# Performance work log

Hardware: AMD Instinct MI355X
Metric: run time of the kernel (lower is better)

Reference implementation:

```python
import jax, jax.numpy as jnp
import numpy as np

B, S, T, D, N, V = 16, 4, 1000, 256, 8192, 50000
EPS = 2.220446049250313e-16  # sys.float_info.epsilon


def setup_inputs() -> dict:
    key = jax.random.key(0)
    ks = jax.random.split(key, 10)
    spks = jax.random.normal(ks[0], (B, S, T, D), jnp.float32)   # frame-level speaker vectors
    ys = jax.random.uniform(ks[1], (B, T, S), jnp.float32)        # predictions (unused in math)
    ts = jax.random.uniform(ks[2], (B, T, S), jnp.float32)        # soft targets / weights
    ss = jax.random.randint(ks[3], (B, S), 0, N)                  # candidate index per speaker
    sigmas = jnp.argsort(jax.random.uniform(ks[4], (B, S)), axis=1)  # per-sample permutation
    ns = jax.random.randint(ks[5], (B, N), 0, V)                  # candidate speaker ids
    ilens = jax.random.randint(ks[6], (B,), T // 2, T + 1)        # valid frame counts
    table = jax.random.normal(ks[7], (V, D), jnp.float32)         # nn.Embedding weight
    alpha = jax.random.uniform(ks[8], (), jnp.float32) + 0.5
    beta = jax.random.uniform(ks[9], (), jnp.float32) + 0.5
    return {"spks": spks, "ys": ys, "ts": ts, "ss": ss, "sigmas": sigmas,
            "ns": ns, "ilens": ilens, "table": table, "alpha": alpha, "beta": beta}


def reference(spks, ys, ts, ss, sigmas, ns, ilens, table, alpha, beta):
    # frame validity mask [B,T]
    mask = (jnp.arange(T)[None, :] < ilens[:, None]).astype(spks.dtype)
    # per-frame L2 normalize speaker vectors: [B,S,T,D]
    nspk = spks / jnp.linalg.norm(spks, axis=-1, keepdims=True)
    # weights w[b,s,t] = ts[b, t, sigma[b,s]]
    w_raw = jnp.take_along_axis(ts, sigmas[:, None, :], axis=2)  # [B,T,S]
    w_raw = jnp.transpose(w_raw, (0, 2, 1))                      # [B,S,T]
    w = w_raw * mask[:, None, :]
    # weighted average over valid frames, then normalize: [B,S,D]
    wavg = jnp.einsum('bst,bstd->bsd', w, nspk)
    e = wavg / jnp.linalg.norm(wavg, axis=-1, keepdims=True)
    # gather + normalize candidate embeddings: [B,N,D]
    emb = table[ns]
    emb = emb / jnp.linalg.norm(emb, axis=-1, keepdims=True)
    # squared euclidean distance between unit vectors: dist^2 = 2 - 2 cos
    dist2 = jnp.maximum(2.0 - 2.0 * jnp.einsum('bsd,bnd->bsn', e, emb), 0.0)
    d = jnp.maximum(alpha, EPS) * dist2 + beta                   # [B,S,N]
    logp = jax.nn.log_softmax(-d, axis=-1)
    idx = jnp.take_along_axis(ss, sigmas, axis=1)                # s[sigma[spkid]] -> [B,S]
    loss_bs = -jnp.take_along_axis(logp, idx[:, :, None], axis=-1)[..., 0]  # [B,S]
    # speaker active iff sum of rounded targets over valid frames > 0
    active = jnp.sum(jnp.round(w_raw) * mask[:, None, :], axis=-1) > 0
    loss_bs = jnp.where(active, loss_bs, 0.0)
    return jnp.mean(loss_bs)
```

## Files before the change

### kernel.cpp

```cpp
#include <hip/hip_runtime.h>
#include <math.h>

#define B_ 16
#define S_ 4
#define T_ 1000
#define D_ 256
#define N_ 8192
#define V_ 50000

constexpr int NC1 = 20;
constexpr int TC1 = (T_ + NC1 - 1) / NC1;
constexpr int NCSE = 32;
constexpr int CPSE = N_ / NCSE;
constexpr int GNB  = (V_ + 63) / 64;

constexpr size_t OFF_W   = 0;
constexpr size_t OFF_CNT = OFF_W   + (size_t)64*NC1*D_;
constexpr size_t OFF_E   = OFF_CNT + (size_t)64*NC1;
constexpr size_t OFF_IDX = OFF_E   + (size_t)64*D_;
constexpr size_t OFF_ACT = OFF_IDX + 64;
constexpr size_t OFF_DT  = OFF_ACT + 64;
constexpr size_t OFF_SE  = OFF_DT  + 64;
constexpr size_t OFF_DOT = OFF_SE  + (size_t)B_*NCSE*S_;
constexpr size_t OFF_N2  = OFF_DOT + (size_t)V_*64;
constexpr size_t WS_FULL_FLOATS = OFF_N2 + V_;

typedef __attribute__((ext_vector_type(8))) short bf16x8;
typedef __attribute__((ext_vector_type(4))) float f32x4;

__device__ inline unsigned short f2bf(float x) {
    unsigned int u = __float_as_uint(x);
    return (unsigned short)((u + 0x7FFFu + ((u >> 16) & 1u)) >> 16);
}

__global__ __launch_bounds__(256) void k1_frames(
    const float* __restrict__ spks, const float* __restrict__ ts,
    const int* __restrict__ sigmas, const int* __restrict__ ilens,
    float* __restrict__ Wp, float* __restrict__ Cp)
{
    const int blk   = blockIdx.x;
    const int bs    = blk / NC1;
    const int chunk = blk % NC1;
    const int b = bs / S_, s = bs % S_;
    const int sig  = sigmas[b * S_ + s];
    const int ilen = ilens[b];
    const int t0 = chunk * TC1;
    int t1 = t0 + TC1; if (t1 > T_) t1 = T_; if (t1 > ilen) t1 = ilen;

    const int wid  = threadIdx.x >> 6;
    const int lane = threadIdx.x & 63;

    float4 acc = make_float4(0.f, 0.f, 0.f, 0.f);
    float  cnt = 0.f;
    const float* base = spks + (size_t)bs * T_ * D_;

    for (int t = t0 + wid; t < t1; t += 4) {
        float4 v = *(const float4*)(base + (size_t)t * D_ + lane * 4);
        float n2 = v.x * v.x + v.y * v.y + v.z * v.z + v.w * v.w;
        #pragma unroll
        for (int o = 32; o >= 1; o >>= 1) n2 += __shfl_xor(n2, o, 64);
        const float w = ts[(b * T_ + t) * S_ + sig];
        const float scale = w / sqrtf(n2);
        acc.x += v.x * scale; acc.y += v.y * scale;
        acc.z += v.z * scale; acc.w += v.w * scale;
        if (lane == 0) cnt += rintf(w);
    }

    __shared__ float sacc[4][D_];
    __shared__ float scnt[4];
    sacc[wid][lane * 4 + 0] = acc.x;
    sacc[wid][lane * 4 + 1] = acc.y;
    sacc[wid][lane * 4 + 2] = acc.z;
    sacc[wid][lane * 4 + 3] = acc.w;
    if (lane == 0) scnt[wid] = cnt;
    __syncthreads();

    const int d = threadIdx.x;
    const float sum = sacc[0][d] + sacc[1][d] + sacc[2][d] + sacc[3][d];
    Wp[((size_t)bs * NC1 + chunk) * D_ + d] = sum;
    if (threadIdx.x == 0)
        Cp[(size_t)bs * NC1 + chunk] = scnt[0] + scnt[1] + scnt[2] + scnt[3];
}

__global__ __launch_bounds__(256) void k2_evec(
    const float* __restrict__ Wp, const float* __restrict__ Cp,
    const int* __restrict__ ss, const int* __restrict__ sigmas,
    float* __restrict__ E, int* __restrict__ IDX, float* __restrict__ ACT)
{
    const int bs = blockIdx.x;
    const int d  = threadIdx.x;
    float sum = 0.f;
    for (int c = 0; c < NC1; ++c) sum += Wp[((size_t)bs * NC1 + c) * D_ + d];

    float n2 = sum * sum;
    #pragma unroll
    for (int o = 32; o >= 1; o >>= 1) n2 += __shfl_xor(n2, o, 64);
    __shared__ float wsum[4];
    if ((threadIdx.x & 63) == 0) wsum[threadIdx.x >> 6] = n2;
    __syncthreads();
    const float tot = wsum[0] + wsum[1] + wsum[2] + wsum[3];

    E[(size_t)bs * D_ + d] = sum / sqrtf(tot);

    if (threadIdx.x == 0) {
        float c = 0.f;
        for (int i = 0; i < NC1; ++i) c += Cp[(size_t)bs * NC1 + i];
        ACT[bs] = c;
        const int b = bs / S_, s = bs % S_;
        IDX[bs] = ss[b * S_ + sigmas[b * S_ + s]];
    }
}

__global__ __launch_bounds__(256) void kG_mfma(
    const float* __restrict__ table, const float* __restrict__ E,
    float* __restrict__ dots, float* __restrict__ N2v)
{
    __shared__ unsigned short e_lds[64][264];
    const int tid = threadIdx.x;

    {
        const float4* Ef4 = (const float4*)E;
        for (int idx = tid; idx < 64 * 64; idx += 256) {
            const int bs = idx >> 6, p = idx & 63;
            const float4 v = Ef4[idx];
            unsigned short* dst = &e_lds[bs][p * 4];
            dst[0] = f2bf(v.x); dst[1] = f2bf(v.y);
            dst[2] = f2bf(v.z); dst[3] = f2bf(v.w);
        }
    }
    __syncthreads();

    const int wv = tid >> 6, l = tid & 63;
    const int lr = l & 15;
    const int lk = l >> 4;
    const int v0 = blockIdx.x * 64 + wv * 16;
    const int vr = v0 + lr;
    const int vload = (vr < V_) ? vr : 0;
    const float* __restrict__ rowp = table + (size_t)vload * D_ + 8 * lk;

    f32x4 acc[4] = {{0.f,0.f,0.f,0.f},{0.f,0.f,0.f,0.f},
                    {0.f,0.f,0.f,0.f},{0.f,0.f,0.f,0.f}};
    float n2 = 0.f;

    #pragma unroll
    for (int ks = 0; ks < 8; ++ks) {
        const float4 lo = *(const float4*)(rowp + ks * 32);
        const float4 hi = *(const float4*)(rowp + ks * 32 + 4);
        n2 += lo.x*lo.x + lo.y*lo.y + lo.z*lo.z + lo.w*lo.w
            + hi.x*hi.x + hi.y*hi.y + hi.z*hi.z + hi.w*hi.w;
        bf16x8 a;
        a[0] = (short)f2bf(lo.x); a[1] = (short)f2bf(lo.y);
        a[2] = (short)f2bf(lo.z); a[3] = (short)f2bf(lo.w);
        a[4] = (short)f2bf(hi.x); a[5] = (short)f2bf(hi.y);
        a[6] = (short)f2bf(hi.z); a[7] = (short)f2bf(hi.w);
        #pragma unroll
        for (int cg = 0; cg < 4; ++cg) {
            const bf16x8 bf = *(const bf16x8*)&e_lds[cg * 16 + lr][ks * 32 + 8 * lk];
            acc[cg] = __builtin_amdgcn_mfma_f32_16x16x32_bf16(a, bf, acc[cg], 0, 0, 0);
        }
    }

    n2 += __shfl_xor(n2, 16, 64);
    n2 += __shfl_xor(n2, 32, 64);
    if (l < 16 && vr < V_) N2v[vr] = n2;

    #pragma unroll
    for (int cg = 0; cg < 4; ++cg) {
        #pragma unroll
        for (int r = 0; r < 4; ++r) {
            const int v = v0 + 4 * lk + r;
            if (v < V_) dots[(size_t)v * 64 + cg * 16 + lr] = acc[cg][r];
        }
    }
}

__global__ __launch_bounds__(256) void k3b_soft(
    const float* __restrict__ dots, const float* __restrict__ N2v,
    const int* __restrict__ ns, const int* __restrict__ IDX,
    const float* __restrict__ alpha_p, const float* __restrict__ beta_p,
    float* __restrict__ DT, float* __restrict__ SE)
{
    const int b     = blockIdx.x / NCSE;
    const int chunk = blockIdx.x % NCSE;
    const int tid   = threadIdx.x;
    const int wid   = tid >> 6;
    const int lane  = tid & 63;

    const float alpha = fmaxf(alpha_p[0], 2.220446049250313e-16f);
    const float beta  = beta_p[0];

    const int n  = chunk * CPSE + tid;
    const int id = ns[b * N_ + n];
    const float4 c4 = *(const float4*)(dots + (size_t)id * 64 + b * 4);
    const float invn = rsqrtf(N2v[id]);
    const float cos4[4] = {c4.x * invn, c4.y * invn, c4.z * invn, c4.w * invn};

    float se[S_];
    #pragma unroll
    for (int s2 = 0; s2 < S_; ++s2) {
        const float dist2 = fmaxf(2.f - 2.f * cos4[s2], 0.f);
        const float dd    = alpha * dist2 + beta;
        se[s2] = expf(-dd);
        if (n == IDX[b * S_ + s2]) DT[b * S_ + s2] = dd;
    }

    #pragma unroll
    for (int o = 1; o <= 32; o <<= 1) {
        #pragma unroll
        for (int s2 = 0; s2 < S_; ++s2) se[s2] += __shfl_xor(se[s2], o, 64);
    }
    __shared__ float sse[4][S_];
    if (lane == 0) {
        #pragma unroll
        for (int s2 = 0; s2 < S_; ++s2) sse[wid][s2] = se[s2];
    }
    __syncthreads();
    if (tid < S_)
        SE[((size_t)b * NCSE + chunk) * S_ + tid] =
            sse[0][tid] + sse[1][tid] + sse[2][tid] + sse[3][tid];
}

__global__ __launch_bounds__(256) void k3_gather(
    const float* __restrict__ table, const int* __restrict__ ns,
    const float* __restrict__ E, const int* __restrict__ IDX,
    const float* __restrict__ alpha_p, const float* __restrict__ beta_p,
    float* __restrict__ DT, float* __restrict__ SE)
{
    const int b     = blockIdx.x / NCSE;
    const int chunk = blockIdx.x % NCSE;
    const int wid  = threadIdx.x >> 6;
    const int lane = threadIdx.x & 63;

    __shared__ float e_s[S_ * D_];
    for (int i = threadIdx.x; i < S_ * D_; i += 256)
        e_s[i] = E[(size_t)b * S_ * D_ + i];
    __syncthreads();

    const float alpha = fmaxf(alpha_p[0], 2.220446049250313e-16f);
    const float beta  = beta_p[0];
    int tgt[S_];
    #pragma unroll
    for (int s2 = 0; s2 < S_; ++s2) tgt[s2] = IDX[b * S_ + s2];

    const int n  = chunk * CPSE + threadIdx.x;
    const int id = ns[b * N_ + n];
    const float* __restrict__ row = table + (size_t)id * D_;

    float n2 = 0.f;
    float dp[S_] = {0.f, 0.f, 0.f, 0.f};
    #pragma unroll 4
    for (int d = 0; d < D_; d += 4) {
        const float4 v = *(const float4*)(row + d);
        n2 += v.x * v.x + v.y * v.y + v.z * v.z + v.w * v.w;
        #pragma unroll
        for (int s2 = 0; s2 < S_; ++s2) {
            const float4 e4 = *(const float4*)(e_s + s2 * D_ + d);
            dp[s2] += e4.x * v.x + e4.y * v.y + e4.z * v.z + e4.w * v.w;
        }
    }

    const float invn = 1.f / sqrtf(n2);
    float se[S_];
    #pragma unroll
    for (int s2 = 0; s2 < S_; ++s2) {
        const float cosv  = dp[s2] * invn;
        const float dist2 = fmaxf(2.f - 2.f * cosv, 0.f);
        const float dd    = alpha * dist2 + beta;
        se[s2] = expf(-dd);
        if (n == tgt[s2]) DT[b * S_ + s2] = dd;
    }

    #pragma unroll
    for (int o = 1; o <= 32; o <<= 1) {
        #pragma unroll
        for (int s2 = 0; s2 < S_; ++s2) se[s2] += __shfl_xor(se[s2], o, 64);
    }
    __shared__ float sse[4][S_];
    if (lane == 0) {
        #pragma unroll
        for (int s2 = 0; s2 < S_; ++s2) sse[wid][s2] = se[s2];
    }
    __syncthreads();
    if (threadIdx.x < S_)
        SE[((size_t)b * NCSE + chunk) * S_ + threadIdx.x] =
            sse[0][threadIdx.x] + sse[1][threadIdx.x] +
            sse[2][threadIdx.x] + sse[3][threadIdx.x];
}

__global__ __launch_bounds__(64) void k4_final(
    const float* __restrict__ SE, const float* __restrict__ DT,
    const float* __restrict__ ACT, float* __restrict__ out)
{
    const int bs = threadIdx.x;
    const int b = bs / S_, s = bs % S_;
    double sum = 0.0;
    for (int c = 0; c < NCSE; ++c) sum += (double)SE[((size_t)b * NCSE + c) * S_ + s];
    float loss = DT[bs] + (float)log(sum);
    if (!(ACT[bs] > 0.f)) loss = 0.f;
    float v = loss;
    #pragma unroll
    for (int o = 32; o >= 1; o >>= 1) v += __shfl_xor(v, o, 64);
    if (bs == 0) out[0] = v / 64.f;
}

extern "C" void kernel_launch(void* const* d_in, const int* in_sizes, int n_in,
                              void* d_out, int out_size, void* d_ws, size_t ws_size,
                              hipStream_t stream)
{
    const float* spks   = (const float*)d_in[0];
    const float* ts     = (const float*)d_in[2];
    const int*   ss     = (const int*)  d_in[3];
    const int*   sigmas = (const int*)  d_in[4];
    const int*   ns     = (const int*)  d_in[5];
    const int*   ilens  = (const int*)  d_in[6];
    const float* table  = (const float*)d_in[7];
    const float* alpha  = (const float*)d_in[8];
    const float* beta   = (const float*)d_in[9];
    float* out = (float*)d_out;

    float* ws = (float*)d_ws;
    float* Wp  = ws + OFF_W;
    float* Cp  = ws + OFF_CNT;
    float* E   = ws + OFF_E;
    int*   IDX = (int*)(ws + OFF_IDX);
    float* ACT = ws + OFF_ACT;
    float* DT  = ws + OFF_DT;
    float* SE  = ws + OFF_SE;
    float* DOT = ws + OFF_DOT;
    float* N2v = ws + OFF_N2;

    k1_frames<<<64 * NC1, 256, 0, stream>>>(spks, ts, sigmas, ilens, Wp, Cp);
    k2_evec  <<<64,       256, 0, stream>>>(Wp, Cp, ss, sigmas, E, IDX, ACT);

    if (ws_size >= WS_FULL_FLOATS * sizeof(float)) {
        kG_mfma <<<GNB,       256, 0, stream>>>(table, E, DOT, N2v);
        k3b_soft<<<B_ * NCSE, 256, 0, stream>>>(DOT, N2v, ns, IDX, alpha, beta, DT, SE);
    } else {
        k3_gather<<<B_ * NCSE, 256, 0, stream>>>(table, ns, E, IDX, alpha, beta, DT, SE);
    }
    k4_final <<<1, 64, 0, stream>>>(SE, DT, ACT, out);
}
```

Before: 41.77 us.

## Stage table rows into LDS via async global_load_lds and keep E fragments in registers

The table-dot kernel now loads a 32-row tile of table rows straight into LDS with asynchronous global_load_lds, using an XOR swizzle to avoid bank conflicts. Each wave converts its half of the E columns into bf16 fragments held in registers, while the row tile is split across two wave pairs. This reduces the per-block footprint and doubles the block count, aiming for more memory-level parallelism and occupancy (launch_bounds 256,4). The frame kernel's chunk count is also halved. The costs are that every block redundantly reloads and converts the E matrix from global memory, and register pressure rises from holding 16 bf16x8 fragments.

```diff
diff --git a/kernel.cpp b/kernel.cpp
--- a/kernel.cpp
+++ b/kernel.cpp
@@ -8,11 +8,12 @@
 #define N_ 8192
 #define V_ 50000
 
-constexpr int NC1 = 20;
+constexpr int NC1 = 10;
 constexpr int TC1 = (T_ + NC1 - 1) / NC1;
 constexpr int NCSE = 32;
 constexpr int CPSE = N_ / NCSE;
-constexpr int GNB  = (V_ + 63) / 64;
+constexpr int GROWS = 32;
+constexpr int GNB  = (V_ + GROWS - 1) / GROWS;
 
 constexpr size_t OFF_W   = 0;
 constexpr size_t OFF_CNT = OFF_W   + (size_t)64*NC1*D_;
@@ -28,6 +29,9 @@
 typedef __attribute__((ext_vector_type(8))) short bf16x8;
 typedef __attribute__((ext_vector_type(4))) float f32x4;
 
+#define GLOBAL_AS __attribute__((address_space(1)))
+#define LDS_AS    __attribute__((address_space(3)))
+
 __device__ inline unsigned short f2bf(float x) {
     unsigned int u = __float_as_uint(x);
     return (unsigned short)((u + 0x7FFFu + ((u >> 16) & 1u)) >> 16);
@@ -111,65 +115,87 @@
     }
 }
 
-__global__ __launch_bounds__(256) void kG_mfma(
+__global__ __launch_bounds__(256, 4) void kG_mfma(
     const float* __restrict__ table, const float* __restrict__ E,
     float* __restrict__ dots, float* __restrict__ N2v)
 {
-    __shared__ unsigned short e_lds[64][264];
-    const int tid = threadIdx.x;
-
-    {
-        const float4* Ef4 = (const float4*)E;
-        for (int idx = tid; idx < 64 * 64; idx += 256) {
-            const int bs = idx >> 6, p = idx & 63;
-            const float4 v = Ef4[idx];
-            unsigned short* dst = &e_lds[bs][p * 4];
-            dst[0] = f2bf(v.x); dst[1] = f2bf(v.y);
-            dst[2] = f2bf(v.z); dst[3] = f2bf(v.w);
+    __shared__ float4 a_lds[GROWS * 64];
+    const int tid  = threadIdx.x;
+    const int wid  = tid >> 6;
+    const int lane = tid & 63;
+    const int lr   = lane & 15;
+    const int lk   = lane >> 4;
+    const int rowgrp = wid & 1;
+    const int ch     = wid >> 1;
+    const int v0 = blockIdx.x * GROWS;
+
+    #pragma unroll
+    for (int r8 = 0; r8 < 8; ++r8) {
+        const int r  = wid * 8 + r8;
+        int vr = v0 + r; if (vr >= V_) vr = V_ - 1;
+        const float* src = table + (size_t)vr * D_ + ((lane ^ (r & 7)) << 2);
+        __builtin_amdgcn_global_load_lds(
+            (const GLOBAL_AS void*)src,
+            (LDS_AS void*)(a_lds + r * 64), 16, 0, 0);
+    }
+
+    bf16x8 bfrag[2][8];
+    #pragma unroll
+    for (int cg = 0; cg < 2; ++cg) {
+        const int col = ch * 32 + cg * 16 + lr;
+        const float* ep = E + (size_t)col * D_ + 8 * lk;
+        #pragma unroll
+        for (int ks = 0; ks < 8; ++ks) {
+            const float4 lo = *(const float4*)(ep + ks * 32);
+            const float4 hi = *(const float4*)(ep + ks * 32 + 4);
+            bf16x8 f;
+            f[0] = (short)f2bf(lo.x); f[1] = (short)f2bf(lo.y);
+            f[2] = (short)f2bf(lo.z); f[3] = (short)f2bf(lo.w);
+            f[4] = (short)f2bf(hi.x); f[5] = (short)f2bf(hi.y);
+            f[6] = (short)f2bf(hi.z); f[7] = (short)f2bf(hi.w);
+            bfrag[cg][ks] = f;
         }
     }
     __syncthreads();
 
-    const int wv = tid >> 6, l = tid & 63;
-    const int lr = l & 15;
-    const int lk = l >> 4;
-    const int v0 = blockIdx.x * 64 + wv * 16;
-    const int vr = v0 + lr;
-    const int vload = (vr < V_) ? vr : 0;
-    const float* __restrict__ rowp = table + (size_t)vload * D_ + 8 * lk;
-
-    f32x4 acc[4] = {{0.f,0.f,0.f,0.f},{0.f,0.f,0.f,0.f},
-                    {0.f,0.f,0.f,0.f},{0.f,0.f,0.f,0.f}};
+    const int r    = rowgrp * 16 + lr;
+    const int rsw  = r & 7;
+    const float4* rowb = a_lds + r * 64;
+
+    f32x4 acc[2] = {{0.f,0.f,0.f,0.f},{0.f,0.f,0.f,0.f}};
     float n2 = 0.f;
 
     #pragma unroll
     for (int ks = 0; ks < 8; ++ks) {
-        const float4 lo = *(const float4*)(rowp + ks * 32);
-        const float4 hi = *(const float4*)(rowp + ks * 32 + 4);
-        n2 += lo.x*lo.x + lo.y*lo.y + lo.z*lo.z + lo.w*lo.w
-            + hi.x*hi.x + hi.y*hi.y + hi.z*hi.z + hi.w*hi.w;
+        const int blk = 8 * ks + 2 * lk;
+        const float4 va = rowb[(blk)     ^ rsw];
+        const float4 vb = rowb[(blk + 1) ^ rsw];
+        if (ch == 0)
+            n2 += va.x*va.x + va.y*va.y + va.z*va.z + va.w*va.w
+                + vb.x*vb.x + vb.y*vb.y + vb.z*vb.z + vb.w*vb.w;
         bf16x8 a;
-        a[0] = (short)f2bf(lo.x); a[1] = (short)f2bf(lo.y);
-        a[2] = (short)f2bf(lo.z); a[3] = (short)f2bf(lo.w);
-        a[4] = (short)f2bf(hi.x); a[5] = (short)f2bf(hi.y);
-        a[6] = (short)f2bf(hi.z); a[7] = (short)f2bf(hi.w);
-        #pragma unroll
-        for (int cg = 0; cg < 4; ++cg) {
-            const bf16x8 bf = *(const bf16x8*)&e_lds[cg * 16 + lr][ks * 32 + 8 * lk];
-            acc[cg] = __builtin_amdgcn_mfma_f32_16x16x32_bf16(a, bf, acc[cg], 0, 0, 0);
-        }
-    }
-
-    n2 += __shfl_xor(n2, 16, 64);
-    n2 += __shfl_xor(n2, 32, 64);
-    if (l < 16 && vr < V_) N2v[vr] = n2;
-
-    #pragma unroll
-    for (int cg = 0; cg < 4; ++cg) {
-        #pragma unroll
-        for (int r = 0; r < 4; ++r) {
-            const int v = v0 + 4 * lk + r;
-            if (v < V_) dots[(size_t)v * 64 + cg * 16 + lr] = acc[cg][r];
+        a[0] = (short)f2bf(va.x); a[1] = (short)f2bf(va.y);
+        a[2] = (short)f2bf(va.z); a[3] = (short)f2bf(va.w);
+        a[4] = (short)f2bf(vb.x); a[5] = (short)f2bf(vb.y);
+        a[6] = (short)f2bf(vb.z); a[7] = (short)f2bf(vb.w);
+        #pragma unroll
+        for (int cg = 0; cg < 2; ++cg)
+            acc[cg] = __builtin_amdgcn_mfma_f32_16x16x32_bf16(a, bfrag[cg][ks], acc[cg], 0, 0, 0);
+    }
+
+    if (ch == 0) {
+        n2 += __shfl_xor(n2, 16, 64);
+        n2 += __shfl_xor(n2, 32, 64);
+        const int vr = v0 + rowgrp * 16 + lane;
+        if (lane < 16 && vr < V_) N2v[vr] = n2;
+    }
+
+    #pragma unroll
+    for (int cg = 0; cg < 2; ++cg) {
+        #pragma unroll
+        for (int rr = 0; rr < 4; ++rr) {
+            const int v = v0 + rowgrp * 16 + 4 * lk + rr;
+            if (v < V_) dots[(size_t)v * 64 + ch * 32 + cg * 16 + lr] = acc[cg][rr];
         }
     }
 }
```

Result: slower. 75.58 us (+80.9%).
